# Kernel tuning notes

Hardware: AMD Instinct MI355X
Metric: run time of the kernel (lower is better)

The kernel has to match this reference:

```python
import math
import jax, jax.numpy as jnp
import numpy as np
from jax import lax

B, S, D = 2, 1024, 768
H, E, DH = 12, 8, 64          # n_head, num_experts, head dim
KA = 1                        # top-k experts per head (attention)
KF = 2                        # top-k experts per token (FFN)
DFF = 2048
EMA_DECAY = 0.99
CAP_FACTOR = 1.25
NEG_INF = -1e9


def setup_inputs() -> dict:
    key = jax.random.key(0)
    ks = jax.random.split(key, 16)
    sc = 0.02
    x = jax.random.normal(ks[0], (B, S, D), jnp.float32)
    causal = jnp.tril(jnp.ones((S, S), jnp.float32))
    mask = jnp.where(causal > 0, 0.0, NEG_INF).astype(jnp.float32)
    return {
        "x": x,
        "mask": mask,
        "W_q": jax.random.normal(ks[1], (D, D), jnp.float32) * sc,
        "W_k": jax.random.normal(ks[2], (D, D), jnp.float32) * sc,
        "W_v": jax.random.normal(ks[3], (H, E, DH, DH), jnp.float32) * sc,
        "W_o": jax.random.normal(ks[4], (H, E, DH, DH), jnp.float32) * sc,
        "W_router": jax.random.normal(ks[5], (D, H * E), jnp.float32) * sc,
        "g1": jnp.ones((D,), jnp.float32),
        "b1": jnp.zeros((D,), jnp.float32),
        "g2": jnp.ones((D,), jnp.float32),
        "b2": jnp.zeros((D,), jnp.float32),
        "gate_ff": jax.random.normal(ks[6], (D, E), jnp.float32) * sc,
        "W1": jax.random.normal(ks[7], (E, D, DFF), jnp.float32) * sc,
        "W2": jax.random.normal(ks[8], (E, DFF, D), jnp.float32) * sc,
    }


def layer_norm(x, g, b, eps=1e-5):
    m = jnp.mean(x, -1, keepdims=True)
    v = jnp.var(x, -1, keepdims=True)
    return (x - m) * lax.rsqrt(v + eps) * g + b


def head_switch_attention(x, mask, W_q, W_k, W_v, W_o, W_router):
    b, s, d = x.shape
    q = (x @ W_q).reshape(b, s, H, DH)
    k = (x @ W_k).reshape(b, s, H, DH)
    scores = jnp.einsum("bshd,bthd->bhst", q, k) / math.sqrt(DH) + mask
    p_attn = jax.nn.softmax(scores, axis=-1)          # (B,H,S,S)
    gate_logits = (x @ W_router).reshape(b, s, H, E)
    topk_scores, topk_idx = lax.top_k(gate_logits, KA)  # (B,S,H,KA)
    probs = jax.nn.softmax(topk_scores, axis=-1)
    x_h = x.reshape(b, s, H, DH)
    # value projections for all experts (small d_h x d_h GEMMs)
    v_all = jnp.einsum("bshd,hedf->bshef", x_h, W_v)
    y = jnp.zeros_like(x_h)
    hard_counts = jnp.zeros((H, E), jnp.float32)
    for slot in range(KA):
        oh = jax.nn.one_hot(topk_idx[..., slot], E, dtype=x.dtype)  # (B,S,H,E)
        v_sel = jnp.einsum("bshef,bshe->bshf", v_all, oh)
        # faithful to original einsum 'bhst,hbsd->hbtd' (sums over s)
        attn_out = jnp.einsum("bhst,bshf->bthf", p_attn, v_sel)
        o_all = jnp.einsum("bthf,hefg->btheg", attn_out, W_o)
        o_sel = jnp.einsum("btheg,bthe->bthg", o_all, oh)
        y = y + o_sel * probs[..., slot][..., None]
        hard_counts = hard_counts + lax.stop_gradient(oh).sum((0, 1))
    y = y.reshape(b, s, d)
    # EMA buffers start at zero -> ema = (1-decay)*hard/denom
    ema = hard_counts / (b * s * KA) * (1.0 - EMA_DECAY)
    p_lb = ema / (ema.sum() + 1e-9)
    aux = (p_lb * p_lb).sum() * E * H
    return y, aux


def moe_ffn(x, gate_ff, W1, W2):
    b, s, d = x.shape
    gate_logits = x @ gate_ff                      # (B,S,E), eval: no noise
    topk_scores, topk_idx = lax.top_k(gate_logits, KF)
    probs = jax.nn.softmax(topk_scores, axis=-1)   # (B,S,KF)
    capacity = math.ceil(CAP_FACTOR * (b * s) / E)
    flat_idx = topk_idx.reshape(-1)                # (B*S*KF,)
    oh_flat = jax.nn.one_hot(flat_idx, E, dtype=jnp.float32)
    tokens_so_far = jnp.cumsum(oh_flat, axis=0)
    keep = jnp.take_along_axis(tokens_so_far <= capacity, flat_idx[:, None], axis=1)[:, 0]
    probs = probs * keep.reshape(b, s, KF).astype(probs.dtype)
    probs = probs / (probs.sum(-1, keepdims=True) + 1e-9)
    oh = jax.nn.one_hot(topk_idx, E, dtype=probs.dtype)   # (B,S,KF,E)
    w = (probs[..., None] * oh).sum(2).reshape(b * s, E)  # combined weight per (token, expert)
    xf = x.reshape(b * s, d)
    yf = jnp.zeros_like(xf)
    for e in range(E):
        # scaling applied BEFORE ReLU, matching original x_sel = x * weight
        xe = xf * w[:, e:e + 1]
        yf = yf + jnp.maximum(xe @ W1[e], 0.0) @ W2[e]
    token_ctr = ((probs > 0)[..., None].astype(jnp.float32) * oh).sum((0, 1, 2))
    imp_ctr = (probs[..., None] * oh).sum((0, 1, 2))
    aux = ((token_ctr / token_ctr.sum()) * (imp_ctr / imp_ctr.sum())).sum() * E
    return yf.reshape(b, s, d), aux


def reference(x, mask, W_q, W_k, W_v, W_o, W_router, g1, b1, g2, b2, gate_ff, W1, W2):
    # pre-norm transformer block: x + Attn(LN(x)); x + MoEFFN(LN(x))
    a, aux1 = head_switch_attention(layer_norm(x, g1, b1), mask, W_q, W_k, W_v, W_o, W_router)
    x1 = x + a  # dropout is identity in eval
    f, aux2 = moe_ffn(layer_norm(x1, g2, b2), gate_ff, W1, W2)
    return x1 + f, aux1 + aux2
```

## Files before the change

### kernel.cpp

```cpp
#include <hip/hip_runtime.h>
#include <hip/hip_bf16.h>
#include <cstdint>

typedef __hip_bfloat16 bf16;
typedef __attribute__((ext_vector_type(8))) __bf16 bfrag;
typedef __attribute__((ext_vector_type(4))) float f32x4;

#define B_    2
#define S_    1024
#define D_    768
#define H_    12
#define E_    8
#define DH_   64
#define DFF_  2048
#define CAP_  320
#define CAPP_ 384
#define NTOK  (B_*S_)
#define NTH   (NTOK*H_)
#define QKLD  1536
#define NHE   (H_*E_)

__device__ __forceinline__ void stage16(const bf16* g, bf16* ldsLane){
#if __has_builtin(__builtin_amdgcn_global_load_lds)
  __builtin_amdgcn_global_load_lds((const __attribute__((address_space(1))) unsigned int*)g,
                                   (__attribute__((address_space(3))) unsigned int*)ldsLane, 16, 0, 0);
#else
  *(bfrag*)ldsLane = *(const bfrag*)g;
#endif
}

__global__ __launch_bounds__(256)
void transp_all(const float* __restrict__ Wq, const float* __restrict__ Wk,
                const float* __restrict__ Wr, const float* __restrict__ W1,
                const float* __restrict__ W2,
                bf16* __restrict__ WcatB, float* __restrict__ WrT,
                bf16* __restrict__ WT1, bf16* __restrict__ WT2)
{
  __shared__ float t[128][64];
  int bid = blockIdx.x, tid = threadIdx.x;
  if (bid < 3216){
    const float* src; int N, K, bx, by; bf16* dst;
    if (bid < 72)      {                src = Wq; N=768;  K=768;  bx=bid%12; by=bid/12; dst=WcatB; }
    else if (bid <144) { int r=bid-72;  src = Wk; N=768;  K=768;  bx=r%12;   by=r/12;   dst=WcatB+(long)768*768; }
    else if (bid<1680) { int r=bid-144; int e=r/192; r-=e*192;
                         src = W1+(long)e*768*2048; N=2048; K=768;  bx=r%32; by=r/32;   dst=WT1+(long)e*2048*768; }
    else               { int r=bid-1680; int e=r/192; r-=e*192;
                         src = W2+(long)e*2048*768; N=768;  K=2048; bx=r%12; by=r/12;   dst=WT2+(long)e*768*2048; }
    int n0 = bx*64, k0 = by*128;
    int chunk = tid & 15, rgrp = tid >> 4;
#pragma unroll
    for (int rr=0; rr<8; rr++){
      int row = rr*16 + rgrp;
      float4 v = *(const float4*)(src + (long)(k0+row)*N + n0 + chunk*4);
      *(float4*)&t[row][((chunk ^ (row>>3)) & 15)*4] = v;
    }
    __syncthreads();
#pragma unroll
    for (int it=0; it<4; it++){
      int slot = it*256 + tid;
      int n = slot >> 4, kc = slot & 15;
      union { bfrag f; bf16 h[8]; } o;
#pragma unroll
      for (int i=0;i<8;i++){
        int row = kc*8 + i;
        o.h[i] = __float2bfloat16(t[row][n ^ (kc*4)]);
      }
      *(bfrag*)(dst + (long)(n0+n)*K + k0 + kc*8) = o.f;
    }
  } else {
    int r = bid - 3216;
    int n0 = (r % 3)*32, k0 = (r / 3)*64;
    int chunk = tid & 7, row2 = tid >> 3;
#pragma unroll
    for (int rr=0; rr<2; rr++){
      int row = rr*32 + row2;
      float4 v = *(const float4*)(Wr + (long)(k0+row)*96 + n0 + chunk*4);
      *(float4*)&t[row][chunk*4] = v;
    }
    __syncthreads();
    int chunkw = tid & 15, ng = tid >> 4;
#pragma unroll
    for (int rr=0; rr<2; rr++){
      int n = rr*16 + ng;
      float4 o;
      o.x = t[chunkw*4+0][n]; o.y = t[chunkw*4+1][n];
      o.z = t[chunkw*4+2][n]; o.w = t[chunkw*4+3][n];
      *(float4*)(WrT + (long)(n0+n)*768 + k0 + chunkw*4) = o;
    }
  }
}

__global__ __launch_bounds__(256)
void gemm_bn64(const bf16* __restrict__ A, const bf16* __restrict__ Bt,
               void* __restrict__ C, void* __restrict__ C2,
               int M, int N, int K, long sA, long sB, long sC, int relu, int outBf, int kSplit)
{
  int nwg = gridDim.x*gridDim.y*gridDim.z;
  int bid = blockIdx.x + gridDim.x*(blockIdx.y + gridDim.y*blockIdx.z);
  int nid = (bid & 7)*(nwg >> 3) + (bid >> 3);
  int bx = nid % gridDim.x;
  int t1 = nid / gridDim.x;
  int by = t1 % gridDim.y;
  int bz = t1 / gridDim.y;
  int e  = bz / kSplit, kc = bz - e*kSplit;
  A  += (long)e*sA;
  Bt += (long)e*sB;
  int kLen = K / kSplit, kBase = kc*kLen;
  int m0 = by*128, n0 = bx*64;
  __shared__ bf16 As[2][128*32];
  __shared__ bf16 Bs[2][64*32];
  int tid = threadIdx.x;
  int w = tid >> 6, lane = tid & 63;
  int quad = lane >> 4, l16 = lane & 15;
  int wm = w*32;
  f32x4 acc[2][4] = {};
  int srow = (lane >> 2);
  int gsw  = ((lane & 3) ^ (srow & 3))*8;
  const bf16* aBase = A + (long)m0*K;
  const bf16* bBase = Bt + (long)n0*K;
  int xr = (l16 & 3);
  int nIt = kLen >> 5;
  {
    int k0 = kBase;
#pragma unroll
    for (int j=0;j<2;j++){
      int c = w*2 + j, row = c*16 + srow;
      stage16(aBase + (long)row*K + k0 + gsw, As[0] + c*512 + lane*8);
    }
    int rowb = w*16 + srow;
    stage16(bBase + (long)rowb*K + k0 + gsw, Bs[0] + w*512 + lane*8);
  }
  int cur = 0;
  for (int it=0; it<nIt; ++it){
    __syncthreads();
    if (it+1 < nIt){
      int k0 = kBase + (it+1)*32;
      int nb = cur^1;
#pragma unroll
      for (int j=0;j<2;j++){
        int c = w*2 + j, row = c*16 + srow;
        stage16(aBase + (long)row*K + k0 + gsw, As[nb] + c*512 + lane*8);
      }
      int rowb = w*16 + srow;
      stage16(bBase + (long)rowb*K + k0 + gsw, Bs[nb] + w*512 + lane*8);
    }
    const bf16* Ac = As[cur];
    const bf16* Bc = Bs[cur];
    bfrag af[2], bfv[4];
#pragma unroll
    for (int t=0;t<2;t++) af[t]  = *(const bfrag*)(Ac + (wm + t*16 + l16)*32 + ((quad ^ xr)*8));
#pragma unroll
    for (int t=0;t<4;t++) bfv[t] = *(const bfrag*)(Bc + (t*16 + l16)*32 + ((quad ^ xr)*8));
#pragma unroll
    for (int ti=0;ti<2;ti++)
#pragma unroll
      for (int tj=0;tj<4;tj++)
        acc[ti][tj] = __builtin_amdgcn_mfma_f32_16x16x32_bf16(af[ti], bfv[tj], acc[ti][tj], 0, 0, 0);
    cur ^= 1;
  }
  long zoff = (long)e*sC;
  void* Cp = kc ? C2 : C;
  if (outBf){
    bf16* Cb = (bf16*)Cp + zoff;
#pragma unroll
    for (int ti=0;ti<2;ti++)
#pragma unroll
      for (int tj=0;tj<4;tj++)
#pragma unroll
        for (int r=0;r<4;r++){
          int row = m0 + wm + ti*16 + quad*4 + r;
          int col = n0 + tj*16 + l16;
          float v = acc[ti][tj][r];
          if (relu) v = fmaxf(v, 0.f);
          Cb[(long)row*N + col] = __float2bfloat16(v);
        }
  } else {
    float* Cf = (float*)Cp + zoff;
#pragma unroll
    for (int ti=0;ti<2;ti++)
#pragma unroll
      for (int tj=0;tj<4;tj++)
#pragma unroll
        for (int r=0;r<4;r++){
          int row = m0 + wm + ti*16 + quad*4 + r;
          int col = n0 + tj*16 + l16;
          float v = acc[ti][tj][r];
          if (relu) v = fmaxf(v, 0.f);
          Cf[(long)row*N + col] = v;
        }
  }
}

__global__ __launch_bounds__(256)
void gemm_ffn1(const float* __restrict__ ln2, const bf16* __restrict__ Bt, bf16* __restrict__ C,
               const int* __restrict__ lTok, const float* __restrict__ lW, const int* __restrict__ gCnt)
{
  int nwg = gridDim.x*gridDim.y*gridDim.z;
  int bid = blockIdx.x + gridDim.x*(blockIdx.y + gridDim.y*blockIdx.z);
  int nid = (bid & 7)*(nwg >> 3) + (bid >> 3);
  int bx = nid % gridDim.x;
  int t1 = nid / gridDim.x;
  int by = t1 % gridDim.y;
  int e  = t1 / gridDim.y;
  int m0 = by*128;
  const bf16* bBase = Bt + (long)e*2048*768 + (long)(bx*64)*768;
  __shared__ bf16 As[2][128*32];
  __shared__ bf16 Bs[2][64*32];
  int tid = threadIdx.x;
  int w = tid >> 6, lane = tid & 63;
  int quad = lane >> 4, l16 = lane & 15;
  int wm = w*32;
  f32x4 acc[2][4] = {};
  int srow = (lane >> 2);
  int gsw  = ((lane & 3) ^ (srow & 3))*8;
  int xr = (l16 & 3);
  int cnt = gCnt[e];
  int tokA[2]; float wA[2];
#pragma unroll
  for (int j=0;j<2;j++){
    int row = m0 + (w*2+j)*16 + srow;
    bool live = row < cnt;
    tokA[j] = live ? lTok[e*CAP_ + row] : 0;
    wA[j]   = live ? lW[e*CAP_ + row]   : 0.f;
  }
  const int nIt = 24;
  {
#pragma unroll
    for (int j=0;j<2;j++){
      const float* src = ln2 + (long)tokA[j]*D_ + gsw;
      float4 a0 = *(const float4*)(src);
      float4 a1 = *(const float4*)(src+4);
      union { bfrag f; bf16 h[8]; } o;
      o.h[0]=__float2bfloat16(a0.x*wA[j]); o.h[1]=__float2bfloat16(a0.y*wA[j]);
      o.h[2]=__float2bfloat16(a0.z*wA[j]); o.h[3]=__float2bfloat16(a0.w*wA[j]);
      o.h[4]=__float2bfloat16(a1.x*wA[j]); o.h[5]=__float2bfloat16(a1.y*wA[j]);
      o.h[6]=__float2bfloat16(a1.z*wA[j]); o.h[7]=__float2bfloat16(a1.w*wA[j]);
      *(bfrag*)(As[0] + (w*2+j)*512 + lane*8) = o.f;
    }
    int rowb = w*16 + srow;
    stage16(bBase + (long)rowb*768 + gsw, Bs[0] + w*512 + lane*8);
  }
  int cur = 0;
  for (int it=0; it<nIt; ++it){
    __syncthreads();
    float4 a0[2], a1[2];
    if (it+1 < nIt){
      int k0 = (it+1)*32;
#pragma unroll
      for (int j=0;j<2;j++){
        const float* src = ln2 + (long)tokA[j]*D_ + k0 + gsw;
        a0[j] = *(const float4*)(src);
        a1[j] = *(const float4*)(src+4);
      }
      int rowb = w*16 + srow;
      stage16(bBase + (long)rowb*768 + k0 + gsw, Bs[cur^1] + w*512 + lane*8);
    }
    const bf16* Ac = As[cur];
    const bf16* Bc = Bs[cur];
    bfrag af[2], bfv[4];
#pragma unroll
    for (int t=0;t<2;t++) af[t]  = *(const bfrag*)(Ac + (wm + t*16 + l16)*32 + ((quad ^ xr)*8));
#pragma unroll
    for (int t=0;t<4;t++) bfv[t] = *(const bfrag*)(Bc + (t*16 + l16)*32 + ((quad ^ xr)*8));
#pragma unroll
    for (int ti=0;ti<2;ti++)
#pragma unroll
      for (int tj=0;tj<4;tj++)
        acc[ti][tj] = __builtin_amdgcn_mfma_f32_16x16x32_bf16(af[ti], bfv[tj], acc[ti][tj], 0, 0, 0);
    if (it+1 < nIt){
      int nb = cur^1;
#pragma unroll
      for (int j=0;j<2;j++){
        union { bfrag f; bf16 h[8]; } o;
        o.h[0]=__float2bfloat16(a0[j].x*wA[j]); o.h[1]=__float2bfloat16(a0[j].y*wA[j]);
        o.h[2]=__float2bfloat16(a0[j].z*wA[j]); o.h[3]=__float2bfloat16(a0[j].w*wA[j]);
        o.h[4]=__float2bfloat16(a1[j].x*wA[j]); o.h[5]=__float2bfloat16(a1[j].y*wA[j]);
        o.h[6]=__float2bfloat16(a1[j].z*wA[j]); o.h[7]=__float2bfloat16(a1[j].w*wA[j]);
        *(bfrag*)(As[nb] + (w*2+j)*512 + lane*8) = o.f;
      }
    }
    cur ^= 1;
  }
  bf16* Cb = C + (long)e*CAPP_*DFF_;
#pragma unroll
  for (int ti=0;ti<2;ti++)
#pragma unroll
    for (int tj=0;tj<4;tj++)
#pragma unroll
      for (int r=0;r<4;r++){
        int row = m0 + wm + ti*16 + quad*4 + r;
        int col = bx*64 + tj*16 + l16;
        Cb[(long)row*DFF_ + col] = __float2bfloat16(fmaxf(acc[ti][tj][r], 0.f));
      }
}

__global__ __launch_bounds__(256)
void ln_kernel(const float* __restrict__ src, const float* __restrict__ g, const float* __restrict__ bb,
               float* __restrict__ dstF, bf16* __restrict__ dstB,
               const float* __restrict__ gateW, float* __restrict__ glog2)
{
  int row = blockIdx.x, tid = threadIdx.x;
  __shared__ float red[256];
  __shared__ float gsum[4][E_];
  float v[3];
#pragma unroll
  for (int j=0;j<3;j++) v[j] = src[(long)row*D_ + tid + j*256];
  float s = v[0]+v[1]+v[2];
  red[tid]=s; __syncthreads();
  for (int o=128;o>0;o>>=1){ if(tid<o) red[tid]+=red[tid+o]; __syncthreads(); }
  float mean = red[0]*(1.0f/D_);
  __syncthreads();
  float sq = 0.f;
#pragma unroll
  for (int j=0;j<3;j++){ float d=v[j]-mean; sq += d*d; }
  red[tid]=sq; __syncthreads();
  for (int o=128;o>0;o>>=1){ if(tid<o) red[tid]+=red[tid+o]; __syncthreads(); }
  float rstd = rsqrtf(red[0]*(1.0f/D_) + 1e-5f);
  float ov[3];
#pragma unroll
  for (int j=0;j<3;j++){
    int d = tid + j*256;
    float o = (v[j]-mean)*rstd*g[d] + bb[d];
    ov[j] = o;
    dstF[(long)row*D_+d] = o;
    if (dstB) dstB[(long)row*D_+d] = __float2bfloat16(o);
  }
  if (gateW){
    float gp[E_] = {};
#pragma unroll
    for (int j=0;j<3;j++){
      int d = tid + j*256;
      const float* gw = gateW + (long)d*E_;
#pragma unroll
      for (int e=0;e<E_;e++) gp[e] += ov[j]*gw[e];
    }
#pragma unroll
    for (int off=1; off<64; off<<=1)
#pragma unroll
      for (int e=0;e<E_;e++) gp[e] += __shfl_xor(gp[e], off);
    if ((tid & 63) == 0)
#pragma unroll
      for (int e=0;e<E_;e++) gsum[tid>>6][e] = gp[e];
    __syncthreads();
    if (tid < E_)
      glog2[(long)row*E_ + tid] = gsum[0][tid]+gsum[1][tid]+gsum[2][tid]+gsum[3][tid];
  }
}

#define RTOK 4
__global__ __launch_bounds__(768)
void router_argmax(const float* __restrict__ ln1, const float* __restrict__ WrT,
                   int* __restrict__ eidx, int* __restrict__ gHist,
                   int* __restrict__ hCnt, int* __restrict__ hList)
{
  int tok0 = blockIdx.x*RTOK;
  int tid = threadIdx.x;
  int col = tid >> 3, seg = tid & 7;
  __shared__ float xrow[RTOK][D_];
  __shared__ float logits[RTOK][96];
  for (int i=tid; i<RTOK*D_; i+=768){
    int t = i / D_, dpos = i - t*D_;
    xrow[t][dpos] = ln1[(long)(tok0+t)*D_ + dpos];
  }
  __syncthreads();
  const float* wrow = WrT + (long)col*D_;
  float acc[RTOK] = {};
#pragma unroll
  for (int j=0;j<24;j++){
    int dbase = j*32 + seg*4;
    float4 w = *(const float4*)(wrow + dbase);
#pragma unroll
    for (int t=0;t<RTOK;t++){
      float4 xv = *(const float4*)(&xrow[t][dbase]);
      acc[t] += xv.x*w.x + xv.y*w.y + xv.z*w.z + xv.w*w.w;
    }
  }
#pragma unroll
  for (int off=1; off<8; off<<=1)
#pragma unroll
    for (int t=0;t<RTOK;t++) acc[t] += __shfl_xor(acc[t], off);
  if (seg == 0)
#pragma unroll
    for (int t=0;t<RTOK;t++) logits[t][col] = acc[t];
  __syncthreads();
  if (tid < RTOK*H_){
    int t = tid / H_, h = tid % H_;
    const float* p = &logits[t][h*8];
    float best = p[0]; int bi = 0;
#pragma unroll
    for (int e=1;e<8;e++){ float v=p[e]; if (v > best){ best=v; bi=e; } }
    int tok = tok0 + t;
    eidx[tok*H_ + h] = bi;
    atomicAdd(&gHist[h*E_ + bi], 1);
    int he = h*E_ + bi;
    int pos = atomicAdd(&hCnt[he], 1);
    hList[he*NTOK + pos] = tok;
  }
}

__global__ __launch_bounds__(256)
void vsel_b(const float* __restrict__ ln1, const float* __restrict__ Wv,
            const int* __restrict__ hCnt, const int* __restrict__ hList,
            bf16* __restrict__ vT)
{
  int he = blockIdx.x;
  int h = he >> 3;
  __shared__ float Ws[DH_*DH_];
  __shared__ float xsh[4][DH_];
  int tid = threadIdx.x;
  const float* W = Wv + (long)he*DH_*DH_;
  for (int i=tid; i<DH_*DH_; i+=256) Ws[i] = W[i];
  int cnt = hCnt[he];
  __syncthreads();
  int w = tid >> 6, lane = tid & 63;
  const int* lst = hList + (long)he*NTOK;
  for (int i = blockIdx.y*4 + w; i < cnt; i += 32){
    int tok = lst[i];
    int b = tok >> 10, s = tok & 1023;
    xsh[w][lane] = ln1[(long)tok*D_ + h*DH_ + lane];
    float acc = 0.f;
#pragma unroll 8
    for (int d=0; d<DH_; d++) acc += xsh[w][d]*Ws[d*DH_ + lane];
    vT[((long)(b*H_+h)*DH_ + lane)*S_ + s] = __float2bfloat16(acc);
  }
}

__global__ __launch_bounds__(256)
void attn_stats_mfma(const bf16* __restrict__ qkB, float* __restrict__ gM, float* __restrict__ gL)
{
  int h = blockIdx.y, b = blockIdx.z;
  int tid = threadIdx.x;
  int w = tid >> 6, lane = tid & 63;
  int quad = lane >> 4, l16 = lane & 15;
  int x7 = l16 & 7;
  __shared__ bf16 ldsQ[64*64];
  __shared__ bf16 ldsK[2][64*64];
  const bf16* kbase = qkB + ((long)(b*S_))*QKLD + 768 + h*DH_;
  for (int half=0; half<2; half++){
    int s0 = (half ? (S_/64 - 1 - blockIdx.x) : blockIdx.x)*64;
    __syncthreads();
    const bf16* qbase = qkB + ((long)(b*S_ + s0))*QKLD + h*DH_;
#pragma unroll
    for (int j=0;j<2;j++){
      int c = j*256 + tid;
      int row = c >> 3;
      int gs = ((c & 7) ^ (row & 7))*8;
      stage16(qbase + (long)row*QKLD + gs, ldsQ + c*8);
      stage16(kbase + (long)row*QKLD + gs, ldsK[0] + c*8);
    }
    float m_ln[4] = {-1e30f,-1e30f,-1e30f,-1e30f};
    float l_ln[4] = {0.f,0.f,0.f,0.f};
    int ttEnd = s0 >> 6;
    int cur = 0;
    for (int tt=0; tt<=ttEnd; tt++){
      __syncthreads();
      if (tt < ttEnd){
#pragma unroll
        for (int j=0;j<2;j++){
          int c = j*256 + tid;
          int row = c >> 3;
          int gs = ((c & 7) ^ (row & 7))*8;
          stage16(kbase + (long)((tt+1)*64 + row)*QKLD + gs, ldsK[cur^1] + c*8);
        }
      }
      const bf16* Kc = ldsK[cur];
      bfrag af0 = *(const bfrag*)(ldsQ + (w*16 + l16)*64 + ((quad     ^ x7)*8));
      bfrag af1 = *(const bfrag*)(ldsQ + (w*16 + l16)*64 + (((quad+4) ^ x7)*8));
      f32x4 cfr[4];
#pragma unroll
      for (int j=0;j<4;j++){
        bfrag b0 = *(const bfrag*)(Kc + (j*16 + l16)*64 + ((quad     ^ x7)*8));
        bfrag b1 = *(const bfrag*)(Kc + (j*16 + l16)*64 + (((quad+4) ^ x7)*8));
        f32x4 z = {};
        z = __builtin_amdgcn_mfma_f32_16x16x32_bf16(af0, b0, z, 0,0,0);
        z = __builtin_amdgcn_mfma_f32_16x16x32_bf16(af1, b1, z, 0,0,0);
        cfr[j] = z;
      }
#pragma unroll
      for (int r=0;r<4;r++){
        int s_g = s0 + w*16 + quad*4 + r;
        float v0 = (tt*64      + l16 <= s_g) ? cfr[0][r]*0.125f : -1e30f;
        float v1 = (tt*64 + 16 + l16 <= s_g) ? cfr[1][r]*0.125f : -1e30f;
        float v2 = (tt*64 + 32 + l16 <= s_g) ? cfr[2][r]*0.125f : -1e30f;
        float v3 = (tt*64 + 48 + l16 <= s_g) ? cfr[3][r]*0.125f : -1e30f;
        float mt = fmaxf(fmaxf(v0,v1), fmaxf(v2,v3));
        float mn = fmaxf(m_ln[r], mt);
        l_ln[r] = l_ln[r]*__expf(m_ln[r]-mn)
                + ((__expf(v0-mn)+__expf(v1-mn)) + (__expf(v2-mn)+__expf(v3-mn)));
        m_ln[r] = mn;
      }
      cur ^= 1;
    }
#pragma unroll
    for (int r=0;r<4;r++){
      float mf = m_ln[r];
#pragma unroll
      for (int mm=1; mm<16; mm<<=1) mf = fmaxf(mf, __shfl_xor(mf, mm));
      float lf = l_ln[r]*__expf(m_ln[r]-mf);
#pragma unroll
      for (int mm=1; mm<16; mm<<=1) lf += __shfl_xor(lf, mm);
      if (l16 == 0){
        long basei = ((long)(b*H_ + h))*S_ + s0 + w*16 + quad*4 + r;
        gM[basei] = mf; gL[basei] = lf;
      }
    }
  }
}

__global__ __launch_bounds__(256)
void attn_pv(const bf16* __restrict__ qkB, const bf16* __restrict__ vT,
             const float* __restrict__ gM, const float* __restrict__ gL, float* __restrict__ aoH)
{
  int h = blockIdx.y, b = blockIdx.z;
  int bh = b*H_ + h;
  int tid = threadIdx.x;
  int w = tid >> 6, lane = tid & 63;
  int quad = lane >> 4, l16 = lane & 15;
  int x7 = l16 & 7;
  __shared__ bf16 ldsK[64*64];
  __shared__ bf16 ldsQ[2][64*64];
  __shared__ bf16 ldsV[2][64*64];
  __shared__ bf16 ldsS[64*72];
  __shared__ float smx[2][64], sli[2][64];
  const bf16* qbase = qkB + ((long)(b*S_))*QKLD + h*DH_;
  const bf16* vbase = vT + ((long)bh*DH_)*S_;
  for (int half=0; half<2; half++){
    int t0 = (half ? (S_/64 - 1 - blockIdx.x) : blockIdx.x)*64;
    __syncthreads();
    const bf16* kbase = qkB + ((long)(b*S_ + t0))*QKLD + 768 + h*DH_;
    int sb0 = t0 >> 6;
#pragma unroll
    for (int j=0;j<2;j++){
      int c = j*256 + tid;
      int row = c >> 3;
      int gs = ((c & 7) ^ (row & 7))*8;
      stage16(kbase + (long)row*QKLD + gs, ldsK + c*8);
      stage16(qbase + (long)(sb0*64 + row)*QKLD + gs, ldsQ[0] + c*8);
      stage16(vbase + (long)row*S_ + sb0*64 + gs, ldsV[0] + c*8);
    }
    if (tid < 64){
      smx[0][tid] = gM[(long)bh*S_ + sb0*64 + tid];
      sli[0][tid] = 1.0f / gL[(long)bh*S_ + sb0*64 + tid];
    }
    f32x4 accO[4] = {};
    int cur = 0;
    for (int sb = sb0; sb < S_/64; sb++){
      __syncthreads();
      if (sb+1 < S_/64){
        int nb = cur^1;
#pragma unroll
        for (int j=0;j<2;j++){
          int c = j*256 + tid;
          int row = c >> 3;
          int gs = ((c & 7) ^ (row & 7))*8;
          stage16(qbase + (long)((sb+1)*64 + row)*QKLD + gs, ldsQ[nb] + c*8);
          stage16(vbase + (long)row*S_ + (sb+1)*64 + gs, ldsV[nb] + c*8);
        }
        if (tid < 64){
          smx[nb][tid] = gM[(long)bh*S_ + (sb+1)*64 + tid];
          sli[nb][tid] = 1.0f / gL[(long)bh*S_ + (sb+1)*64 + tid];
        }
      }
      const bf16* Qc = ldsQ[cur];
      const bf16* Vc = ldsV[cur];
      bfrag af0 = *(const bfrag*)(ldsK + (w*16 + l16)*64 + ((quad     ^ x7)*8));
      bfrag af1 = *(const bfrag*)(ldsK + (w*16 + l16)*64 + (((quad+4) ^ x7)*8));
      f32x4 cs[4];
#pragma unroll
      for (int j=0;j<4;j++){
        bfrag b0 = *(const bfrag*)(Qc + (j*16 + l16)*64 + ((quad     ^ x7)*8));
        bfrag b1 = *(const bfrag*)(Qc + (j*16 + l16)*64 + (((quad+4) ^ x7)*8));
        f32x4 z = {};
        z = __builtin_amdgcn_mfma_f32_16x16x32_bf16(af0, b0, z, 0,0,0);
        z = __builtin_amdgcn_mfma_f32_16x16x32_bf16(af1, b1, z, 0,0,0);
        cs[j] = z;
      }
#pragma unroll
      for (int j=0;j<4;j++)
#pragma unroll
        for (int r=0;r<4;r++){
          int t_loc = w*16 + quad*4 + r;
          int s_loc = j*16 + l16;
          float wgt = ((t0 + t_loc) <= (sb*64 + s_loc))
                    ? __expf(cs[j][r]*0.125f - smx[cur][s_loc])*sli[cur][s_loc] : 0.f;
          ldsS[t_loc*72 + s_loc] = __float2bfloat16(wgt);
        }
      bfrag pa0 = *(const bfrag*)(ldsS + (w*16 + l16)*72 + quad*8);
      bfrag pa1 = *(const bfrag*)(ldsS + (w*16 + l16)*72 + 32 + quad*8);
#pragma unroll
      for (int j=0;j<4;j++){
        bfrag b0 = *(const bfrag*)(Vc + (j*16 + l16)*64 + ((quad     ^ x7)*8));
        bfrag b1 = *(const bfrag*)(Vc + (j*16 + l16)*64 + (((quad+4) ^ x7)*8));
        accO[j] = __builtin_amdgcn_mfma_f32_16x16x32_bf16(pa0, b0, accO[j], 0,0,0);
        accO[j] = __builtin_amdgcn_mfma_f32_16x16x32_bf16(pa1, b1, accO[j], 0,0,0);
      }
      cur ^= 1;
    }
#pragma unroll
    for (int j=0;j<4;j++)
#pragma unroll
      for (int r=0;r<4;r++){
        int t_loc = w*16 + quad*4 + r;
        int f = j*16 + l16;
        aoH[((long)bh*S_ + t0 + t_loc)*DH_ + f] = accO[j][r];
      }
  }
}

__global__ __launch_bounds__(256)
void oproj_b(const float* __restrict__ aoH, const float* __restrict__ Wo,
             const int* __restrict__ hCnt, const int* __restrict__ hList,
             const float* __restrict__ x, float* __restrict__ x1)
{
  int he = blockIdx.x;
  int h = he >> 3;
  __shared__ float Ws[DH_*DH_];
  __shared__ float xsh[4][DH_];
  int tid = threadIdx.x;
  const float* W = Wo + (long)he*DH_*DH_;
  for (int i=tid; i<DH_*DH_; i+=256) Ws[i] = W[i];
  int cnt = hCnt[he];
  __syncthreads();
  int w = tid >> 6, lane = tid & 63;
  const int* lst = hList + (long)he*NTOK;
  for (int i = blockIdx.y*4 + w; i < cnt; i += 32){
    int tok = lst[i];
    int b = tok >> 10, s = tok & 1023;
    xsh[w][lane] = aoH[((long)(b*H_+h)*S_ + s)*DH_ + lane];
    float acc = 0.f;
#pragma unroll 8
    for (int f=0; f<DH_; f++) acc += xsh[w][f]*Ws[f*DH_ + lane];
    long idx = (long)tok*D_ + h*DH_ + lane;
    x1[idx] = x[idx] + acc;
  }
}

__global__ __launch_bounds__(256)
void route_kernel(const float* __restrict__ glog2, const int* __restrict__ gHist,
                  int* __restrict__ gI0, int* __restrict__ gI1,
                  int* __restrict__ gPos0, int* __restrict__ gPos1,
                  int* __restrict__ listTok, float* __restrict__ listW,
                  int* __restrict__ gCnt, float* __restrict__ auxOut)
{
  __shared__ unsigned char sI0[NTOK], sI1[NTOK];
  __shared__ float sP0[NTOK], sP1[NTOK];
  __shared__ short sPos0[NTOK], sPos1[NTOK];
  __shared__ int   sScan[256*E_];
  __shared__ int   sHist[H_*E_];
  __shared__ float sImp[E_];
  __shared__ int   sCnt[E_];
  int tid = threadIdx.x;
  if (tid < E_) sImp[tid] = 0.f;
  if (tid < H_*E_) sHist[tid] = gHist[tid];
  for (int i=tid; i<NTOK; i+=256){
    const float* p = glog2 + (long)i*E_;
    float b0 = p[0]; int e0 = 0;
#pragma unroll
    for (int e=1;e<E_;e++){ float vv=p[e]; if (vv > b0){ b0=vv; e0=e; } }
    float b1v = -1e30f; int e1 = 0;
#pragma unroll
    for (int e=0;e<E_;e++){ if (e==e0) continue; float vv=p[e]; if (vv > b1v){ b1v=vv; e1=e; } }
    float ex = __expf(b1v - b0);
    float inv = 1.f/(1.f + ex);
    sI0[i] = (unsigned char)e0; sI1[i] = (unsigned char)e1;
    sP0[i] = inv; sP1[i] = ex*inv;
    gI0[i] = e0; gI1[i] = e1;
  }
  __syncthreads();
  {
    int myCnt[E_] = {};
#pragma unroll
    for (int j=0;j<16;j++){
      int i = tid*16 + j;
      int tok = i >> 1;
      int e = (i & 1) ? (int)sI1[tok] : (int)sI0[tok];
      myCnt[e]++;
    }
#pragma unroll
    for (int e=0;e<E_;e++) sScan[tid*E_+e] = myCnt[e];
    __syncthreads();
    for (int off=1; off<256; off<<=1){
      int v[E_];
      if (tid >= off){
#pragma unroll
        for (int e=0;e<E_;e++) v[e] = sScan[(tid-off)*E_+e];
      }
      __syncthreads();
      if (tid >= off){
#pragma unroll
        for (int e=0;e<E_;e++) sScan[tid*E_+e] += v[e];
      }
      __syncthreads();
    }
    int pref[E_];
#pragma unroll
    for (int e=0;e<E_;e++) pref[e] = tid ? sScan[(tid-1)*E_+e] : 0;
#pragma unroll
    for (int j=0;j<16;j++){
      int i = tid*16 + j;
      int tok = i >> 1;
      int e = (i & 1) ? (int)sI1[tok] : (int)sI0[tok];
      int pos = pref[e]++;
      short p = (pos < CAP_) ? (short)pos : (short)-1;
      if (i & 1) sPos1[tok] = p; else sPos0[tok] = p;
    }
    if (tid < E_){
      int cnt = sScan[255*E_ + tid];
      sCnt[tid] = cnt < CAP_ ? cnt : CAP_;
      gCnt[tid] = sCnt[tid];
    }
  }
  __syncthreads();
  for (int i=tid; i<NTOK; i+=256){
    int e0 = sI0[i], e1 = sI1[i];
    int p0i = sPos0[i], p1i = sPos1[i];
    float k0 = p0i >= 0 ? 1.f : 0.f, k1 = p1i >= 0 ? 1.f : 0.f;
    float p0 = sP0[i], p1 = sP1[i];
    float denom = p0*k0 + p1*k1 + 1e-9f;
    float w0 = p0*k0/denom, w1 = p1*k1/denom;
    if (p0i >= 0){ listTok[e0*CAP_+p0i] = i; listW[e0*CAP_+p0i] = w0; atomicAdd(&sImp[e0], w0); }
    if (p1i >= 0){ listTok[e1*CAP_+p1i] = i; listW[e1*CAP_+p1i] = w1; atomicAdd(&sImp[e1], w1); }
    gPos0[i] = p0i; gPos1[i] = p1i;
  }
  __syncthreads();
  if (tid == 0){
    float tot = 0.f;
    for (int i=0;i<H_*E_;i++) tot += (float)sHist[i]*(1.0f/NTOK)*0.01f;
    float a1 = 0.f;
    for (int i=0;i<H_*E_;i++){
      float p = ((float)sHist[i]*(1.0f/NTOK)*0.01f)/(tot + 1e-9f);
      a1 += p*p;
    }
    a1 *= (float)(H_*E_);
    float tcs = 0.f, ims = 0.f;
    for (int e=0;e<E_;e++){ tcs += (float)sCnt[e]; ims += sImp[e]; }
    float a2 = 0.f;
    for (int e=0;e<E_;e++) a2 += ((float)sCnt[e]/tcs)*(sImp[e]/ims);
    a2 *= (float)E_;
    auxOut[0] = a1 + a2;
  }
}

__global__ __launch_bounds__(256)
void combine_kernel(const float* __restrict__ x1,
                    const float* __restrict__ Ya, const float* __restrict__ Yb,
                    const int* __restrict__ gI0, const int* __restrict__ gI1,
                    const int* __restrict__ gPos0, const int* __restrict__ gPos1,
                    float* __restrict__ out)
{
  int i = blockIdx.x;
  int tid = threadIdx.x;
  int p0 = gPos0[i], p1 = gPos1[i];
  int e0 = gI0[i],  e1 = gI1[i];
  long off0 = (long)(e0*CAPP_ + (p0 >= 0 ? p0 : 0))*D_;
  long off1 = (long)(e1*CAPP_ + (p1 >= 0 ? p1 : 0))*D_;
  const float* y0a = Ya + off0; const float* y0b = Yb + off0;
  const float* y1a = Ya + off1; const float* y1b = Yb + off1;
  for (int d=tid; d<D_; d+=256){
    float v = x1[(long)i*D_+d];
    if (p0 >= 0) v += y0a[d] + y0b[d];
    if (p1 >= 0) v += y1a[d] + y1b[d];
    out[(long)i*D_+d] = v;
  }
}

extern "C" void kernel_launch(void* const* d_in, const int* in_sizes, int n_in,
                              void* d_out, int out_size, void* d_ws, size_t ws_size,
                              hipStream_t stream)
{
  const float* x    = (const float*)d_in[0];
  const float* W_q  = (const float*)d_in[2];
  const float* W_k  = (const float*)d_in[3];
  const float* W_v  = (const float*)d_in[4];
  const float* W_o  = (const float*)d_in[5];
  const float* W_r  = (const float*)d_in[6];
  const float* g1   = (const float*)d_in[7];
  const float* b1   = (const float*)d_in[8];
  const float* g2   = (const float*)d_in[9];
  const float* b2   = (const float*)d_in[10];
  const float* gate = (const float*)d_in[11];
  const float* W1   = (const float*)d_in[12];
  const float* W2   = (const float*)d_in[13];
  float* out = (float*)d_out;

  float* wsf = (float*)d_ws;
  const long oX1   = 0;
  const long oLnF  = 1572864;
  const long oLnB  = 3145728;
  const long oWcat = 3932160;
  const long oWrT  = 4521984;
  const long oHist = 4595712;
  const long oHCnt = 4595808;
  const long oGM   = 4718592;
  const long oGL   = 4743168;
  const long oEidx = 4767744;
  const long oGlg2 = 4792320;
  const long oI0   = 4808704;
  const long oI1   = 4810752;
  const long oP0   = 4812800;
  const long oP1   = 4814848;
  const long oLT   = 4816896;
  const long oLW   = 4819456;
  const long oCnt  = 4822016;
  const long SB    = 4822528;
  const long oWT1  = SB + 12976128;
  const long oWT2  = oWT1 + 6291456;
  const long TOTAL = oWT2 + 6291456;
  if (ws_size < (size_t)TOTAL*4) return;

  float* x1    = wsf + oX1;
  float* lnbF  = wsf + oLnF;
  bf16*  lnbB  = (bf16*)(wsf + oLnB);
  bf16*  WcatB = (bf16*)(wsf + oWcat);
  float* WrT   = wsf + oWrT;
  int*   gHist = (int*)(wsf + oHist);
  int*   hCnt  = (int*)(wsf + oHCnt);
  float* gM    = wsf + oGM;
  float* gL    = wsf + oGL;
  int*   eidx  = (int*)(wsf + oEidx);
  float* glog2 = wsf + oGlg2;
  int*   gI0   = (int*)(wsf + oI0);
  int*   gI1   = (int*)(wsf + oI1);
  int*   gPos0 = (int*)(wsf + oP0);
  int*   gPos1 = (int*)(wsf + oP1);
  int*   lTok  = (int*)(wsf + oLT);
  float* lW    = wsf + oLW;
  int*   gCnt  = (int*)(wsf + oCnt);
  bf16*  qkB   = (bf16*)(wsf + SB);
  bf16*  vT    = (bf16*)(wsf + SB + 1572864);
  float* aoH   = wsf + SB + 2359296;
  int*   hList = (int*)(wsf + SB + 3932160);
  bf16*  Hid   = (bf16*)(wsf + SB + 7471104);
  float* Yexp  = wsf + SB + 10616832;
  float* YexpB = wsf + oLnF;
  bf16*  WT1   = (bf16*)(wsf + oWT1);
  bf16*  WT2   = (bf16*)(wsf + oWT2);

  hipMemsetAsync(gHist, 0, 2*NHE*sizeof(int), stream);
  transp_all<<<3252,256,0,stream>>>(W_q, W_k, W_r, W1, W2, WcatB, WrT, WT1, WT2);

  ln_kernel<<<NTOK,256,0,stream>>>(x, g1, b1, lnbF, lnbB, nullptr, nullptr);
  gemm_bn64<<<dim3(24,16,1),256,0,stream>>>(lnbB, WcatB, qkB, nullptr, 2048, QKLD, 768, 0,0,0, 0, 1, 1);
  router_argmax<<<NTOK/RTOK,768,0,stream>>>(lnbF, WrT, eidx, gHist, hCnt, hList);
  vsel_b<<<dim3(NHE,8,1),256,0,stream>>>(lnbF, W_v, hCnt, hList, vT);
  attn_stats_mfma<<<dim3(S_/128,H_,B_),256,0,stream>>>(qkB, gM, gL);
  attn_pv<<<dim3(S_/128,H_,B_),256,0,stream>>>(qkB, vT, gM, gL, aoH);
  oproj_b<<<dim3(NHE,8,1),256,0,stream>>>(aoH, W_o, hCnt, hList, x, x1);

  ln_kernel<<<NTOK,256,0,stream>>>(x1, g2, b2, lnbF, nullptr, gate, glog2);
  route_kernel<<<1,256,0,stream>>>(glog2, gHist, gI0,gI1,gPos0,gPos1, lTok,lW,gCnt, out + (size_t)NTOK*D_);
  gemm_ffn1<<<dim3(32,3,8),256,0,stream>>>(lnbF, WT1, Hid, lTok, lW, gCnt);
  gemm_bn64<<<dim3(12,3,16),256,0,stream>>>(Hid, WT2, Yexp, YexpB, CAPP_, 768, 2048,
                                            (long)CAPP_*2048, (long)768*2048, (long)CAPP_*768, 0, 0, 2);
  combine_kernel<<<NTOK,256,0,stream>>>(x1, Yexp, YexpB, gI0,gI1,gPos0,gPos1, out);
}
```

Before: 395.6 us.

## Fuse FFN weight transpose into attention-stats kernel to overlap with attention

Moves the W1/W2 fp32-to-bf16 transposition blocks out of the upfront transpose kernel and appends them as extra blocks (grid z 2..33) of the attention statistics kernel, so the bandwidth-heavy weight conversion runs alongside the compute-bound attention blocks. The attention-stats shared memory is now a single 32KB buffer reused by both block types. The upfront kernel only handles Wq/Wk/Wr. The attention kernel's LDS footprint grows from 24KB to 32KB, which may reduce occupancy, and its blocks now share the GPU with memory-bound transpose blocks.

After: 382.2 us. -3.4%, faster.

```diff
diff --git a/kernel.cpp b/kernel.cpp
--- a/kernel.cpp
+++ b/kernel.cpp
@@ -29,46 +29,44 @@
 #endif
 }
 
-__global__ __launch_bounds__(256)
-void transp_all(const float* __restrict__ Wq, const float* __restrict__ Wk,
-                const float* __restrict__ Wr, const float* __restrict__ W1,
-                const float* __restrict__ W2,
-                bf16* __restrict__ WcatB, float* __restrict__ WrT,
-                bf16* __restrict__ WT1, bf16* __restrict__ WT2)
+__device__ __forceinline__ void transp_tile_bf16(const float* __restrict__ src, bf16* __restrict__ dst,
+                                                 int N, int K, int n0, int k0, int tid, float (*t)[64])
+{
+  int chunk = tid & 15, rgrp = tid >> 4;
+#pragma unroll
+  for (int rr=0; rr<8; rr++){
+    int row = rr*16 + rgrp;
+    float4 v = *(const float4*)(src + (long)(k0+row)*N + n0 + chunk*4);
+    *(float4*)&t[row][((chunk ^ (row>>3)) & 15)*4] = v;
+  }
+  __syncthreads();
+#pragma unroll
+  for (int it=0; it<4; it++){
+    int slot = it*256 + tid;
+    int n = slot >> 4, kc = slot & 15;
+    union { bfrag f; bf16 h[8]; } o;
+#pragma unroll
+    for (int i=0;i<8;i++){
+      int row = kc*8 + i;
+      o.h[i] = __float2bfloat16(t[row][n ^ (kc*4)]);
+    }
+    *(bfrag*)(dst + (long)(n0+n)*K + k0 + kc*8) = o.f;
+  }
+}
+
+__global__ __launch_bounds__(256)
+void transp_qkr(const float* __restrict__ Wq, const float* __restrict__ Wk,
+                const float* __restrict__ Wr, bf16* __restrict__ WcatB, float* __restrict__ WrT)
 {
   __shared__ float t[128][64];
   int bid = blockIdx.x, tid = threadIdx.x;
-  if (bid < 3216){
-    const float* src; int N, K, bx, by; bf16* dst;
-    if (bid < 72)      {                src = Wq; N=768;  K=768;  bx=bid%12; by=bid/12; dst=WcatB; }
-    else if (bid <144) { int r=bid-72;  src = Wk; N=768;  K=768;  bx=r%12;   by=r/12;   dst=WcatB+(long)768*768; }
-    else if (bid<1680) { int r=bid-144; int e=r/192; r-=e*192;
-                         src = W1+(long)e*768*2048; N=2048; K=768;  bx=r%32; by=r/32;   dst=WT1+(long)e*2048*768; }
-    else               { int r=bid-1680; int e=r/192; r-=e*192;
-                         src = W2+(long)e*2048*768; N=768;  K=2048; bx=r%12; by=r/12;   dst=WT2+(long)e*768*2048; }
-    int n0 = bx*64, k0 = by*128;
-    int chunk = tid & 15, rgrp = tid >> 4;
-#pragma unroll
-    for (int rr=0; rr<8; rr++){
-      int row = rr*16 + rgrp;
-      float4 v = *(const float4*)(src + (long)(k0+row)*N + n0 + chunk*4);
-      *(float4*)&t[row][((chunk ^ (row>>3)) & 15)*4] = v;
-    }
-    __syncthreads();
-#pragma unroll
-    for (int it=0; it<4; it++){
-      int slot = it*256 + tid;
-      int n = slot >> 4, kc = slot & 15;
-      union { bfrag f; bf16 h[8]; } o;
-#pragma unroll
-      for (int i=0;i<8;i++){
-        int row = kc*8 + i;
-        o.h[i] = __float2bfloat16(t[row][n ^ (kc*4)]);
-      }
-      *(bfrag*)(dst + (long)(n0+n)*K + k0 + kc*8) = o.f;
-    }
+  if (bid < 144){
+    const float* src; bf16* dst; int r;
+    if (bid < 72){ src = Wq; dst = WcatB; r = bid; }
+    else         { src = Wk; dst = WcatB + (long)768*768; r = bid - 72; }
+    transp_tile_bf16(src, dst, 768, 768, (r%12)*64, (r/12)*128, tid, t);
   } else {
-    int r = bid - 3216;
+    int r = bid - 144;
     int n0 = (r % 3)*32, k0 = (r / 3)*64;
     int chunk = tid & 7, row2 = tid >> 3;
 #pragma unroll
@@ -426,15 +424,30 @@
 }
 
 __global__ __launch_bounds__(256)
-void attn_stats_mfma(const bf16* __restrict__ qkB, float* __restrict__ gM, float* __restrict__ gL)
-{
+void attn_stats_mfma(const bf16* __restrict__ qkB, float* __restrict__ gM, float* __restrict__ gL,
+                     const float* __restrict__ W1, const float* __restrict__ W2,
+                     bf16* __restrict__ WT1, bf16* __restrict__ WT2)
+{
+  __shared__ __align__(16) char smem[32768];
+  int tid = threadIdx.x;
+  if (blockIdx.z >= 2){
+    int flat = (blockIdx.z - 2)*96 + blockIdx.y*8 + blockIdx.x;
+    const float* src; int N, K, bx, by; bf16* dst;
+    if (flat < 1536){ int e = flat/192, r = flat - e*192;
+      src = W1 + (long)e*768*2048; N = 2048; K = 768;  bx = r % 32; by = r / 32;
+      dst = WT1 + (long)e*2048*768;
+    } else { int f2 = flat - 1536; int e = f2/192, r = f2 - e*192;
+      src = W2 + (long)e*2048*768; N = 768;  K = 2048; bx = r % 12; by = r / 12;
+      dst = WT2 + (long)e*768*2048;
+    }
+    transp_tile_bf16(src, dst, N, K, bx*64, by*128, tid, (float(*)[64])smem);
+    return;
+  }
+  bf16* ldsQ = (bf16*)smem;
   int h = blockIdx.y, b = blockIdx.z;
-  int tid = threadIdx.x;
   int w = tid >> 6, lane = tid & 63;
   int quad = lane >> 4, l16 = lane & 15;
   int x7 = l16 & 7;
-  __shared__ bf16 ldsQ[64*64];
-  __shared__ bf16 ldsK[2][64*64];
   const bf16* kbase = qkB + ((long)(b*S_))*QKLD + 768 + h*DH_;
   for (int half=0; half<2; half++){
     int s0 = (half ? (S_/64 - 1 - blockIdx.x) : blockIdx.x)*64;
@@ -446,7 +459,7 @@
       int row = c >> 3;
       int gs = ((c & 7) ^ (row & 7))*8;
       stage16(qbase + (long)row*QKLD + gs, ldsQ + c*8);
-      stage16(kbase + (long)row*QKLD + gs, ldsK[0] + c*8);
+      stage16(kbase + (long)row*QKLD + gs, (bf16*)(smem + 8192) + c*8);
     }
     float m_ln[4] = {-1e30f,-1e30f,-1e30f,-1e30f};
     float l_ln[4] = {0.f,0.f,0.f,0.f};
@@ -455,15 +468,16 @@
     for (int tt=0; tt<=ttEnd; tt++){
       __syncthreads();
       if (tt < ttEnd){
+        bf16* Kn = (bf16*)(smem + 8192 + ((cur^1) << 13));
 #pragma unroll
         for (int j=0;j<2;j++){
           int c = j*256 + tid;
           int row = c >> 3;
           int gs = ((c & 7) ^ (row & 7))*8;
-          stage16(kbase + (long)((tt+1)*64 + row)*QKLD + gs, ldsK[cur^1] + c*8);
+          stage16(kbase + (long)((tt+1)*64 + row)*QKLD + gs, Kn + c*8);
         }
       }
-      const bf16* Kc = ldsK[cur];
+      const bf16* Kc = (const bf16*)(smem + 8192 + (cur << 13));
       bfrag af0 = *(const bfrag*)(ldsQ + (w*16 + l16)*64 + ((quad     ^ x7)*8));
       bfrag af1 = *(const bfrag*)(ldsQ + (w*16 + l16)*64 + (((quad+4) ^ x7)*8));
       f32x4 cfr[4];
@@ -836,14 +850,14 @@
   bf16*  WT1   = (bf16*)(wsf + oWT1);
   bf16*  WT2   = (bf16*)(wsf + oWT2);
 
-  hipMemsetAsync(gHist, 0, 2*NHE*sizeof(int), stream);
-  transp_all<<<3252,256,0,stream>>>(W_q, W_k, W_r, W1, W2, WcatB, WrT, WT1, WT2);
+  (void)hipMemsetAsync(gHist, 0, 2*NHE*sizeof(int), stream);
+  transp_qkr<<<180,256,0,stream>>>(W_q, W_k, W_r, WcatB, WrT);
 
   ln_kernel<<<NTOK,256,0,stream>>>(x, g1, b1, lnbF, lnbB, nullptr, nullptr);
   gemm_bn64<<<dim3(24,16,1),256,0,stream>>>(lnbB, WcatB, qkB, nullptr, 2048, QKLD, 768, 0,0,0, 0, 1, 1);
   router_argmax<<<NTOK/RTOK,768,0,stream>>>(lnbF, WrT, eidx, gHist, hCnt, hList);
   vsel_b<<<dim3(NHE,8,1),256,0,stream>>>(lnbF, W_v, hCnt, hList, vT);
-  attn_stats_mfma<<<dim3(S_/128,H_,B_),256,0,stream>>>(qkB, gM, gL);
+  attn_stats_mfma<<<dim3(S_/128,H_,2+32),256,0,stream>>>(qkB, gM, gL, W1, W2, WT1, WT2);
   attn_pv<<<dim3(S_/128,H_,B_),256,0,stream>>>(qkB, vT, gM, gL, aoH);
   oproj_b<<<dim3(NHE,8,1),256,0,stream>>>(aoH, W_o, hCnt, hList, x, x1);
 
```
